# Performance work log

Hardware: AMD Instinct MI355X
Metric: run time of the kernel (lower is better)

The kernel has to match this reference:

```python
import jax, jax.numpy as jnp
import numpy as np

NUM_HEADS = 12


def setup_inputs() -> dict:
    key = jax.random.key(0)
    k0, k1, k2 = jax.random.split(key, 3)
    B, S, D = 2, 2048, 1536
    scale = 1.0 / np.sqrt(D)
    return {
        "hidden_states": jax.random.normal(k0, (B, S, D), dtype=jnp.float32),
        "W_fc": jax.random.normal(k1, (D, D), dtype=jnp.float32) * scale,
        "b_fc": jnp.zeros((D,), dtype=jnp.float32),
        "W_proj": jax.random.normal(k2, (D, D), dtype=jnp.float32) * scale,
        "b_proj": jnp.zeros((D,), dtype=jnp.float32),
    }


def reference(hidden_states, W_fc, b_fc, W_proj, b_proj):
    B, S, D = hidden_states.shape
    H = NUM_HEADS
    hd = D // H
    # value_states: [B, H, S, hd] (key_states == value_states in the original)
    v = (hidden_states @ W_fc.T + b_fc).reshape(B, S, H, hd).transpose(0, 2, 1, 3)
    # Uniform-weight causal sliding-window attention, window_h = 2^(h+1)-1.
    i = jnp.arange(S)[:, None]          # query pos
    j = jnp.arange(S)[None, :]          # key pos
    w = (2 ** jnp.arange(1, H + 1, dtype=jnp.int32) - 1)[:, None, None]  # [H,1,1]
    mask = (j <= i) & (j >= i - w + 1)                                    # [H,S,S]
    valid_len = jnp.minimum(i + 1, w).astype(v.dtype)                     # [H,S,1]
    attn = jnp.where(mask, 1.0 / valid_len, 0.0)                          # [H,S,S]
    # [H,S,S] x [B,H,S,hd] -> [B,S,H,hd] -> [B,S,D]
    out = jnp.einsum("hqk,bhkd->bqhd", attn, v).reshape(B, S, D)
    attn_weights = jnp.broadcast_to(attn[None], (B, H, S, S))
    return out @ W_proj.T + b_proj, attn_weights
```

## Files before the change

kernel.cpp:

```cpp
#include <hip/hip_runtime.h>
#include <hip/hip_bf16.h>

#define S_LEN   2048
#define DMODEL  1536
#define NBATCH  2
#define NHEADS  12
#define MROWS   (NBATCH * S_LEN)
#define NCHUNK  16
#define CHUNK   128

typedef unsigned short u16;
typedef __attribute__((ext_vector_type(8))) short bf16x8;
typedef __attribute__((ext_vector_type(4))) float f32x4;

__device__ __forceinline__ u16 f2bf(float x) {
  unsigned u = __float_as_uint(x);
  u += 0x7fffu + ((u >> 16) & 1u);
  return (u16)(u >> 16);
}

__global__ void cvt_f32_to_bf16(const float4* __restrict__ src,
                                ushort4* __restrict__ dst, int n4) {
  int t = blockIdx.x * blockDim.x + threadIdx.x;
  if (t >= n4) return;
  float4 f = src[t];
  ushort4 o;
  o.x = f2bf(f.x); o.y = f2bf(f.y); o.z = f2bf(f.z); o.w = f2bf(f.w);
  dst[t] = o;
}

__device__ __forceinline__ void gld_lds16(u16* lds, const u16* g) {
  __builtin_amdgcn_global_load_lds(
      (const __attribute__((address_space(1))) unsigned int*)g,
      (__attribute__((address_space(3))) unsigned int*)lds, 16, 0, 0);
}

__global__ __launch_bounds__(256)
void gemm_bt_bias(const u16* __restrict__ A, const u16* __restrict__ B,
                  const float* __restrict__ bias, float* __restrict__ C,
                  int Mdim, int Ndim, int Kdim) {
  __shared__ __align__(16) u16 As[128 * 32];
  __shared__ __align__(16) u16 Bs[128 * 32];

  const int tid  = threadIdx.x;
  const int wave = tid >> 6;
  const int lane = tid & 63;
  const int l15  = lane & 15;
  const int quad = lane >> 4;
  const int bm = blockIdx.y * 128;
  const int bn = blockIdx.x * 128;
  const int wm = (wave >> 1) * 64;
  const int wn = (wave & 1) * 64;

  f32x4 acc[4][4] = {};

  const int srow = wave * 32 + (lane >> 2);
  const int skk  = (lane & 3) * 8;
  const u16* gA = A + (size_t)(bm + srow) * Kdim + skk;
  const u16* gB = B + (size_t)(bn + srow) * Kdim + skk;
  u16* lA = &As[(wave * 32) * 32];
  u16* lB = &Bs[(wave * 32) * 32];
  const size_t rstep16 = (size_t)16 * Kdim;

  for (int k0 = 0; k0 < Kdim; k0 += 32) {
    gld_lds16(lA,           gA + k0);
    gld_lds16(lA + 16 * 32, gA + k0 + rstep16);
    gld_lds16(lB,           gB + k0);
    gld_lds16(lB + 16 * 32, gB + k0 + rstep16);
    __syncthreads();

    bf16x8 af[4], bfr[4];
#pragma unroll
    for (int i = 0; i < 4; ++i)
      af[i] = *(const bf16x8*)&As[(wm + i * 16 + l15) * 32 + quad * 8];
#pragma unroll
    for (int j = 0; j < 4; ++j)
      bfr[j] = *(const bf16x8*)&Bs[(wn + j * 16 + l15) * 32 + quad * 8];
#pragma unroll
    for (int i = 0; i < 4; ++i)
#pragma unroll
      for (int j = 0; j < 4; ++j)
        acc[i][j] = __builtin_amdgcn_mfma_f32_16x16x32_bf16(af[i], bfr[j], acc[i][j], 0, 0, 0);
    __syncthreads();
  }

  const int r0 = quad * 4;
#pragma unroll
  for (int j = 0; j < 4; ++j) {
    const int col = bn + wn + j * 16 + l15;
    const float bj = bias[col];
#pragma unroll
    for (int i = 0; i < 4; ++i) {
      const int row = bm + wm + i * 16 + r0;
#pragma unroll
      for (int r = 0; r < 4; ++r)
        C[(size_t)(row + r) * Ndim + col] = acc[i][j][r] + bj;
    }
  }
}

__global__ void chunk_sum(const float* __restrict__ v, float* __restrict__ cs) {
  int t = blockIdx.x * blockDim.x + threadIdx.x;
  int d = t % DMODEL;
  int c = (t / DMODEL) % NCHUNK;
  int b = t / (DMODEL * NCHUNK);
  const float* p = v + ((size_t)b * S_LEN + (size_t)c * CHUNK) * DMODEL + d;
  float s = 0.f;
#pragma unroll 8
  for (int r = 0; r < CHUNK; ++r) s += p[(size_t)r * DMODEL];
  cs[t] = s;
}

__global__ void scan_apply(float* __restrict__ v, const float* __restrict__ cs) {
  int t = blockIdx.x * blockDim.x + threadIdx.x;
  int d = t % DMODEL;
  int c = (t / DMODEL) % NCHUNK;
  int b = t / (DMODEL * NCHUNK);
  float base = 0.f;
  for (int cc = 0; cc < c; ++cc)
    base += cs[((size_t)b * NCHUNK + cc) * DMODEL + d];
  float* p = v + ((size_t)b * S_LEN + (size_t)c * CHUNK) * DMODEL + d;
  float run = base;
#pragma unroll 8
  for (int r = 0; r < CHUNK; ++r) {
    run += p[(size_t)r * DMODEL];
    p[(size_t)r * DMODEL] = run;
  }
}

__global__ void winavg_bf16(const float* __restrict__ P, u16* __restrict__ A2) {
  int t = blockIdx.x * blockDim.x + threadIdx.x;
  int d = t % DMODEL;
  int m = t / DMODEL;
  int i = m & (S_LEN - 1);
  int b = m >> 11;
  int h = d >> 7;
  int w = (2 << h) - 1;
  int len = min(i + 1, w);
  float s = P[(size_t)m * DMODEL + d];
  int jl = i - len;
  if (jl >= 0) s -= P[((size_t)b * S_LEN + jl) * DMODEL + d];
  A2[t] = f2bf(s * (1.0f / (float)len));
}

__global__ void attn_weights_kernel(float4* __restrict__ out4) {
  int t = blockIdx.x * blockDim.x + threadIdx.x;
  int j0 = (t & 511) << 2;
  int i  = (t >> 9) & (S_LEN - 1);
  int bh = t >> 20;
  int h  = bh >= NHEADS ? bh - NHEADS : bh;
  int w  = (2 << h) - 1;
  int len = min(i + 1, w);
  float inv = 1.0f / (float)len;
  int lo = i - w + 1;
  float4 r;
  r.x = (j0     <= i && j0     >= lo) ? inv : 0.f;
  r.y = (j0 + 1 <= i && j0 + 1 >= lo) ? inv : 0.f;
  r.z = (j0 + 2 <= i && j0 + 2 >= lo) ? inv : 0.f;
  r.w = (j0 + 3 <= i && j0 + 3 >= lo) ? inv : 0.f;
  out4[t] = r;
}

extern "C" void kernel_launch(void* const* d_in, const int* in_sizes, int n_in,
                              void* d_out, int out_size, void* d_ws, size_t ws_size,
                              hipStream_t stream) {
  const float* hidden = (const float*)d_in[0];
  const float* W_fc   = (const float*)d_in[1];
  const float* b_fc   = (const float*)d_in[2];
  const float* W_proj = (const float*)d_in[3];
  const float* b_proj = (const float*)d_in[4];
  float* outp = (float*)d_out;

  char* ws = (char*)d_ws;
  u16*   A16   = (u16*)(ws);
  u16*   Wfc16 = (u16*)(ws + 12582912);
  u16*   Wpj16 = (u16*)(ws + 17301504);
  float* vbuf  = (float*)(ws + 22020096);
  float* csums = (float*)(ws + 47185920);

  cvt_f32_to_bf16<<<6144, 256, 0, stream>>>((const float4*)hidden, (ushort4*)A16, 1572864);
  cvt_f32_to_bf16<<<2304, 256, 0, stream>>>((const float4*)W_fc,   (ushort4*)Wfc16, 589824);
  cvt_f32_to_bf16<<<2304, 256, 0, stream>>>((const float4*)W_proj, (ushort4*)Wpj16, 589824);

  gemm_bt_bias<<<dim3(DMODEL / 128, MROWS / 128), 256, 0, stream>>>(
      A16, Wfc16, b_fc, vbuf, MROWS, DMODEL, DMODEL);

  chunk_sum <<<(NBATCH * NCHUNK * DMODEL) / 256, 256, 0, stream>>>(vbuf, csums);
  scan_apply<<<(NBATCH * NCHUNK * DMODEL) / 256, 256, 0, stream>>>(vbuf, csums);

  winavg_bf16<<<(MROWS * DMODEL) / 256, 256, 0, stream>>>(vbuf, A16);

  gemm_bt_bias<<<dim3(DMODEL / 128, MROWS / 128), 256, 0, stream>>>(
      A16, Wpj16, b_proj, outp, MROWS, DMODEL, DMODEL);

  attn_weights_kernel<<<(NBATCH * NHEADS * S_LEN * S_LEN / 4) / 256, 256, 0, stream>>>(
      (float4*)(outp + (size_t)MROWS * DMODEL));
}
```

Baseline: 557.1 us.

## Fuse chunk sums into GEMM epilogue and merge scan with window average

```diff
diff --git a/kernel.cpp b/kernel.cpp
--- a/kernel.cpp
+++ b/kernel.cpp
@@ -19,14 +19,22 @@
   return (u16)(u >> 16);
 }
 
-__global__ void cvt_f32_to_bf16(const float4* __restrict__ src,
-                                ushort4* __restrict__ dst, int n4) {
+#define N4_HID  1572864
+#define N4_W    589824
+__global__ void cvt_all(const float4* __restrict__ h, const float4* __restrict__ wf,
+                        const float4* __restrict__ wp, ushort4* __restrict__ ho,
+                        ushort4* __restrict__ wfo, ushort4* __restrict__ wpo) {
   int t = blockIdx.x * blockDim.x + threadIdx.x;
-  if (t >= n4) return;
-  float4 f = src[t];
+  const float4* src;
+  ushort4* dst;
+  int idx;
+  if (t < N4_HID)            { src = h;  dst = ho;  idx = t; }
+  else if (t < N4_HID + N4_W){ src = wf; dst = wfo; idx = t - N4_HID; }
+  else                       { src = wp; dst = wpo; idx = t - N4_HID - N4_W; }
+  float4 f = src[idx];
   ushort4 o;
   o.x = f2bf(f.x); o.y = f2bf(f.y); o.z = f2bf(f.z); o.w = f2bf(f.w);
-  dst[t] = o;
+  dst[idx] = o;
 }
 
 __device__ __forceinline__ void gld_lds16(u16* lds, const u16* g) {
@@ -35,12 +43,14 @@
       (__attribute__((address_space(3))) unsigned int*)lds, 16, 0, 0);
 }
 
+template <bool WITH_CSUM>
 __global__ __launch_bounds__(256)
 void gemm_bt_bias(const u16* __restrict__ A, const u16* __restrict__ B,
                   const float* __restrict__ bias, float* __restrict__ C,
-                  int Mdim, int Ndim, int Kdim) {
+                  float* __restrict__ cs, int Ndim, int Kdim) {
   __shared__ __align__(16) u16 As[128 * 32];
   __shared__ __align__(16) u16 Bs[128 * 32];
+  __shared__ float colpart[2][128];
 
   const int tid  = threadIdx.x;
   const int wave = tid >> 6;
@@ -89,58 +99,72 @@
   for (int j = 0; j < 4; ++j) {
     const int col = bn + wn + j * 16 + l15;
     const float bj = bias[col];
+    float s = 0.f;
 #pragma unroll
     for (int i = 0; i < 4; ++i) {
       const int row = bm + wm + i * 16 + r0;
 #pragma unroll
-      for (int r = 0; r < 4; ++r)
-        C[(size_t)(row + r) * Ndim + col] = acc[i][j][r] + bj;
-    }
-  }
-}
-
-__global__ void chunk_sum(const float* __restrict__ v, float* __restrict__ cs) {
+      for (int r = 0; r < 4; ++r) {
+        float cv = acc[i][j][r] + bj;
+        C[(size_t)(row + r) * Ndim + col] = cv;
+        s += cv;
+      }
+    }
+    if (WITH_CSUM) {
+      s += __shfl_xor(s, 16);
+      s += __shfl_xor(s, 32);
+      if (quad == 0) colpart[wm >> 6][wn + j * 16 + l15] = s;
+    }
+  }
+  if (WITH_CSUM) {
+    __syncthreads();
+    if (tid < 128) {
+      const int b = bm >> 11;
+      const int c = (bm & 2047) >> 7;
+      cs[((size_t)b * NCHUNK + c) * DMODEL + bn + tid] =
+          colpart[0][tid] + colpart[1][tid];
+    }
+  }
+}
+
+__global__ void winavg_fused(const float* __restrict__ v, const float* __restrict__ cs,
+                             u16* __restrict__ A2) {
   int t = blockIdx.x * blockDim.x + threadIdx.x;
   int d = t % DMODEL;
   int c = (t / DMODEL) % NCHUNK;
   int b = t / (DMODEL * NCHUNK);
-  const float* p = v + ((size_t)b * S_LEN + (size_t)c * CHUNK) * DMODEL + d;
-  float s = 0.f;
-#pragma unroll 8
-  for (int r = 0; r < CHUNK; ++r) s += p[(size_t)r * DMODEL];
-  cs[t] = s;
-}
-
-__global__ void scan_apply(float* __restrict__ v, const float* __restrict__ cs) {
-  int t = blockIdx.x * blockDim.x + threadIdx.x;
-  int d = t % DMODEL;
-  int c = (t / DMODEL) % NCHUNK;
-  int b = t / (DMODEL * NCHUNK);
-  float base = 0.f;
-  for (int cc = 0; cc < c; ++cc)
-    base += cs[((size_t)b * NCHUNK + cc) * DMODEL + d];
-  float* p = v + ((size_t)b * S_LEN + (size_t)c * CHUNK) * DMODEL + d;
-  float run = base;
-#pragma unroll 8
+  const int h = d >> 7;
+  const int w = (2 << h) - 1;
+  const float* vb = v + (size_t)b * S_LEN * DMODEL + d;
+  const float* csb = cs + (size_t)b * NCHUNK * DMODEL + d;
+
+  const int i0 = c * CHUNK;
+  float lead = 0.f;
+  for (int cc = 0; cc < c; ++cc) lead += csb[(size_t)cc * DMODEL];
+
+  float trail = 0.f;
+  const int tstart = i0 - w;
+  if (tstart > 0) {
+    const int tc = tstart >> 7;
+    for (int cc = 0; cc < tc; ++cc) trail += csb[(size_t)cc * DMODEL];
+#pragma unroll 4
+    for (int r = tc * CHUNK; r < tstart; ++r) trail += vb[(size_t)r * DMODEL];
+  }
+
+  u16* out = A2 + ((size_t)(b * S_LEN + i0)) * DMODEL + d;
+#pragma unroll 4
   for (int r = 0; r < CHUNK; ++r) {
-    run += p[(size_t)r * DMODEL];
-    p[(size_t)r * DMODEL] = run;
-  }
-}
-
-__global__ void winavg_bf16(const float* __restrict__ P, u16* __restrict__ A2) {
-  int t = blockIdx.x * blockDim.x + threadIdx.x;
-  int d = t % DMODEL;
-  int m = t / DMODEL;
-  int i = m & (S_LEN - 1);
-  int b = m >> 11;
-  int h = d >> 7;
-  int w = (2 << h) - 1;
-  int len = min(i + 1, w);
-  float s = P[(size_t)m * DMODEL + d];
-  int jl = i - len;
-  if (jl >= 0) s -= P[((size_t)b * S_LEN + jl) * DMODEL + d];
-  A2[t] = f2bf(s * (1.0f / (float)len));
+    const int i = i0 + r;
+    lead += vb[(size_t)i * DMODEL];
+    float o;
+    if (i < w) {
+      o = lead / (float)(i + 1);
+    } else {
+      trail += vb[(size_t)(i - w) * DMODEL];
+      o = (lead - trail) / (float)w;
+    }
+    out[(size_t)r * DMODEL] = f2bf(o);
+  }
 }
 
 __global__ void attn_weights_kernel(float4* __restrict__ out4) {
@@ -178,20 +202,17 @@
   float* vbuf  = (float*)(ws + 22020096);
   float* csums = (float*)(ws + 47185920);
 
-  cvt_f32_to_bf16<<<6144, 256, 0, stream>>>((const float4*)hidden, (ushort4*)A16, 1572864);
-  cvt_f32_to_bf16<<<2304, 256, 0, stream>>>((const float4*)W_fc,   (ushort4*)Wfc16, 589824);
-  cvt_f32_to_bf16<<<2304, 256, 0, stream>>>((const float4*)W_proj, (ushort4*)Wpj16, 589824);
-
-  gemm_bt_bias<<<dim3(DMODEL / 128, MROWS / 128), 256, 0, stream>>>(
-      A16, Wfc16, b_fc, vbuf, MROWS, DMODEL, DMODEL);
-
-  chunk_sum <<<(NBATCH * NCHUNK * DMODEL) / 256, 256, 0, stream>>>(vbuf, csums);
-  scan_apply<<<(NBATCH * NCHUNK * DMODEL) / 256, 256, 0, stream>>>(vbuf, csums);
-
-  winavg_bf16<<<(MROWS * DMODEL) / 256, 256, 0, stream>>>(vbuf, A16);
-
-  gemm_bt_bias<<<dim3(DMODEL / 128, MROWS / 128), 256, 0, stream>>>(
-      A16, Wpj16, b_proj, outp, MROWS, DMODEL, DMODEL);
+  cvt_all<<<10752, 256, 0, stream>>>((const float4*)hidden, (const float4*)W_fc,
+                                     (const float4*)W_proj, (ushort4*)A16,
+                                     (ushort4*)Wfc16, (ushort4*)Wpj16);
+
+  gemm_bt_bias<true><<<dim3(DMODEL / 128, MROWS / 128), 256, 0, stream>>>(
+      A16, Wfc16, b_fc, vbuf, csums, DMODEL, DMODEL);
+
+  winavg_fused<<<(NBATCH * NCHUNK * DMODEL) / 256, 256, 0, stream>>>(vbuf, csums, A16);
+
+  gemm_bt_bias<false><<<dim3(DMODEL / 128, MROWS / 128), 256, 0, stream>>>(
+      A16, Wpj16, b_proj, outp, nullptr, DMODEL, DMODEL);
 
   attn_weights_kernel<<<(NBATCH * NHEADS * S_LEN * S_LEN / 4) / 256, 256, 0, stream>>>(
       (float4*)(outp + (size_t)MROWS * DMODEL));
```

New measurement: 597.0 us. 7.2% more time.
